# Kernel tuning notes

Measured on AMD Instinct MI355X. Metric: run time of the kernel, lower is better.

The kernel has to match this reference:

```python
import jax, jax.numpy as jnp
import numpy as np

NUM_SAMPLES = 50

def _sample_bezier(cp, t):
    # cp: [4, 2], t: [S, 1] -> [S, 2]
    p0, p1, p2, p3 = cp[0], cp[1], cp[2], cp[3]
    return ((1 - t) ** 3 * p0 + 3 * (1 - t) ** 2 * t * p1
            + 3 * (1 - t) * t ** 2 * p2 + t ** 3 * p3)

def setup_inputs() -> dict:
    key = jax.random.key(0)
    k1, k2, k3 = jax.random.split(key, 3)
    num_strokes = 64
    return {
        "strokes": jax.random.uniform(k1, (num_strokes, 4, 2), dtype=jnp.float32),
        "stroke_widths": jax.random.uniform(k2, (num_strokes,), dtype=jnp.float32) * 2.0 + 1.0,
        "stroke_colors": jax.random.uniform(k3, (num_strokes, 3), dtype=jnp.float32),
        "canvas_size": 512,
    }

def reference(strokes, stroke_widths, stroke_colors, canvas_size):
    H = W = canvas_size
    t = jnp.linspace(0.0, 1.0, NUM_SAMPLES, dtype=strokes.dtype)[:, None]  # [S,1]
    # sample all curves: [num_strokes, S, 2], scaled to pixel coords
    points = jax.vmap(lambda cp: _sample_bezier(cp, t))(strokes) * canvas_size
    coords = jnp.arange(canvas_size, dtype=strokes.dtype)
    yy, xx = jnp.meshgrid(coords, coords, indexing="ij")
    grid = jnp.stack([xx, yy], axis=-1)  # [H, W, 2]

    def composite(canvas, inp):
        pts, width, color = inp  # [S,2], [], [3]
        diff = grid[:, :, None, :] - pts[None, None, :, :]      # [H, W, S, 2]
        dist = jnp.sqrt(jnp.sum(diff * diff, axis=-1))           # [H, W, S]
        min_dist = jnp.min(dist, axis=-1)                        # [H, W]
        alpha = jax.nn.sigmoid((width - min_dist) * 2.0)         # [H, W]
        alpha = alpha[None, None]                                # [1,1,H,W]
        color_map = color[None, :, None, None]                   # [1,3,1,1]
        canvas = canvas * (1.0 - alpha) + color_map * alpha
        return canvas, None

    canvas0 = jnp.ones((1, 3, H, W), dtype=strokes.dtype)
    canvas, _ = jax.lax.scan(composite, canvas0, (points, stroke_widths, stroke_colors))
    return canvas
```

## Files before the change

kernel.cpp:

```cpp
#include <hip/hip_runtime.h>

#define NSTROKES 64
#define NSAMP    50
#define CANVAS   512
#define HW       (CANVAS * CANVAS)
#define TPB      1024
#define SPW      (NSTROKES / 16)
#define LSTRIDE  64

__global__ __launch_bounds__(TPB, 8) void raster_fused_kernel(
    const float* __restrict__ strokes,
    const float* __restrict__ widths,
    const float* __restrict__ colors,
    float* __restrict__ out)
{
    __shared__ __align__(16) float2 slist[NSTROKES * LSTRIDE];
    __shared__ float4 scull[NSTROKES];
    __shared__ float4 scol [NSTROKES];

    const int tid  = threadIdx.x;
    const int wave = tid >> 6;
    const int lane = tid & 63;
    const int px   = tid & 511;
    const int grp  = tid >> 9;
    const int y    = blockIdx.x;
    const float fy = (float)y;

    #pragma unroll
    for (int i = 0; i < SPW; ++i) {
        const int s = wave * SPW + i;

        float4 a = ((const float4*)strokes)[s * 2];
        float4 b = ((const float4*)strokes)[s * 2 + 1];
        const float S = (float)CANVAS;
        float c0x = a.x * S;
        float c1x = 3.0f * (a.z - a.x) * S;
        float c2x = 3.0f * (b.x - 2.0f * a.z + a.x) * S;
        float c3x = (b.z - 3.0f * b.x + 3.0f * a.z - a.x) * S;
        float c0y = a.y * S;
        float c1y = 3.0f * (a.w - a.y) * S;
        float c2y = 3.0f * (b.y - 2.0f * a.w + a.y) * S;
        float c3y = (b.w - 3.0f * b.y + 3.0f * a.w - a.y) * S;

        float w   = widths[s];
        float cut = w + 10.0f;

        float t   = (float)lane * (1.0f / (float)(NSAMP - 1));
        float px_ = fmaf(fmaf(fmaf(c3x, t, c2x), t, c1x), t, c0x);
        float py_ = fmaf(fmaf(fmaf(c3y, t, c2y), t, c1y), t, c0y);

        bool keep = (lane < NSAMP) && (fabsf(py_ - fy) <= cut);
        unsigned long long mask = __ballot(keep);
        int idx = __popcll(mask & ((1ull << lane) - 1ull));
        if (keep) {
            slist[s * LSTRIDE + idx] = make_float2(px_, py_);
        } else if (lane >= NSAMP) {
            slist[s * LSTRIDE + idx + (lane - NSAMP)] = make_float2(1e15f, 1e15f);
        }

        if (mask) {
            float vmn = keep ? px_ : 1e30f;
            float vmx = keep ? px_ : -1e30f;
            #pragma unroll
            for (int off = 32; off; off >>= 1) {
                vmn = fminf(vmn, __shfl_xor(vmn, off));
                vmx = fmaxf(vmx, __shfl_xor(vmx, off));
            }
            if (lane == 0) {
                scull[s] = make_float4(vmn - cut, vmx + cut, w,
                                       (float)__popcll(mask));
                scol [s] = make_float4(colors[3*s], colors[3*s+1],
                                       colors[3*s+2], 0.0f);
            }
        } else if (lane == 0) {
            scull[s] = make_float4(0.0f, 0.0f, w, 0.0f);
        }
    }
    __syncthreads();

    const float fx      = (float)px;
    const float span_lo = (float)((wave & 7) << 6);
    const float span_hi = span_lo + 63.0f;
    const int   sbase   = grp << 5;

    float4 cbl = scull[sbase + (lane & 31)];
    bool alive = (cbl.w > 0.0f) && (cbl.x <= span_hi) && (cbl.y >= span_lo);
    unsigned int live = (unsigned int)__ballot(alive);

    float A = 1.0f, br = 0.0f, bg = 0.0f, bb = 0.0f;

    while (live) {
        const int s0 = sbase + (__ffs(live) - 1);
        live &= live - 1u;
        const bool has1 = (live != 0u);
        const int s1 = has1 ? (sbase + (__ffs(live) - 1)) : s0;
        if (has1) live &= live - 1u;

        float4 cb0  = scull[s0];
        float4 cb1  = scull[s1];
        float4 col0 = scol [s0];
        float4 col1 = scol [s1];
        const int   kc0 = (int)cb0.w;
        const int   kc1 = has1 ? (int)cb1.w : 0;
        const float w0  = cb0.z;
        const float w1  = cb1.z;

        float m0 = 1e30f, m1 = 1e30f;
        const float4* L0 = (const float4*)(slist + s0 * LSTRIDE);
        const float4* L1 = (const float4*)(slist + s1 * LSTRIDE);

        const int kmax = kc0 > kc1 ? kc0 : kc1;
        for (int j = 0; j < kmax; j += 4) {
            if (j < kc0) {
                float4 q0 = L0[(j >> 1)];
                float4 q1 = L0[(j >> 1) + 1];
                float dy0 = fy - q0.y, dy1 = fy - q0.w;
                float dy2 = fy - q1.y, dy3 = fy - q1.w;
                float d0  = fx - q0.x, d1  = fx - q0.z;
                float d2  = fx - q1.x, d3  = fx - q1.z;
                float a01 = fminf(fmaf(d0, d0, dy0*dy0), fmaf(d1, d1, dy1*dy1));
                float a23 = fminf(fmaf(d2, d2, dy2*dy2), fmaf(d3, d3, dy3*dy3));
                m0 = fminf(fminf(a01, a23), m0);
            }
            if (j < kc1) {
                float4 q0 = L1[(j >> 1)];
                float4 q1 = L1[(j >> 1) + 1];
                float dy0 = fy - q0.y, dy1 = fy - q0.w;
                float dy2 = fy - q1.y, dy3 = fy - q1.w;
                float d0  = fx - q0.x, d1  = fx - q0.z;
                float d2  = fx - q1.x, d3  = fx - q1.z;
                float a01 = fminf(fmaf(d0, d0, dy0*dy0), fmaf(d1, d1, dy1*dy1));
                float a23 = fminf(fmaf(d2, d2, dy2*dy2), fmaf(d3, d3, dy3*dy3));
                m1 = fminf(fminf(a01, a23), m1);
            }
        }

        float al0 = __builtin_amdgcn_rcpf(1.0f + __expf(2.0f * (sqrtf(m0) - w0)));
        float al1 = __builtin_amdgcn_rcpf(1.0f + __expf(2.0f * (sqrtf(m1) - w1)));

        A  *= (1.0f - al0);
        br  = fmaf(al0, col0.x - br, br);
        bg  = fmaf(al0, col0.y - bg, bg);
        bb  = fmaf(al0, col0.z - bb, bb);
        if (has1) {
            A  *= (1.0f - al1);
            br  = fmaf(al1, col1.x - br, br);
            bg  = fmaf(al1, col1.y - bg, bg);
            bb  = fmaf(al1, col1.z - bb, bb);
        }
    }

    __syncthreads();
    float4* xfer = (float4*)slist;
    if (grp == 0) {
        xfer[px] = make_float4(A, br, bg, bb);
    }
    __syncthreads();
    if (grp == 1) {
        float4 g0 = xfer[px];
        float cr = fmaf(A, g0.x + g0.y, br);
        float cg = fmaf(A, g0.x + g0.z, bg);
        float cb = fmaf(A, g0.x + g0.w, bb);
        const int base = y * CANVAS + px;
        out[0*HW + base] = cr;
        out[1*HW + base] = cg;
        out[2*HW + base] = cb;
    }
}

extern "C" void kernel_launch(void* const* d_in, const int* in_sizes, int n_in,
                              void* d_out, int out_size, void* d_ws, size_t ws_size,
                              hipStream_t stream) {
    const float* strokes = (const float*)d_in[0];
    const float* widths  = (const float*)d_in[1];
    const float* colors  = (const float*)d_in[2];
    float* out = (float*)d_out;

    raster_fused_kernel<<<dim3(CANVAS), dim3(TPB), 0, stream>>>(
        strokes, widths, colors, out);
}
```

Measured before the change: 18.08 us.

## Bucket kept curve samples by x-span so each wave scans only nearby buckets

```diff
diff --git a/kernel.cpp b/kernel.cpp
--- a/kernel.cpp
+++ b/kernel.cpp
@@ -7,6 +7,7 @@
 #define TPB      1024
 #define SPW      (NSTROKES / 16)
 #define LSTRIDE  64
+#define SOFFP    13
 
 __global__ __launch_bounds__(TPB, 8) void raster_fused_kernel(
     const float* __restrict__ strokes,
@@ -15,8 +16,8 @@
     float* __restrict__ out)
 {
     __shared__ __align__(16) float2 slist[NSTROKES * LSTRIDE];
-    __shared__ float4 scull[NSTROKES];
-    __shared__ float4 scol [NSTROKES];
+    __shared__ unsigned int soff[NSTROKES * SOFFP];
+    __shared__ float4 scol[NSTROKES];
 
     const int tid  = threadIdx.x;
     const int wave = tid >> 6;
@@ -50,42 +51,58 @@
         float py_ = fmaf(fmaf(fmaf(c3y, t, c2y), t, c1y), t, c0y);
 
         bool keep = (lane < NSAMP) && (fabsf(py_ - fy) <= cut);
-        unsigned long long mask = __ballot(keep);
-        int idx = __popcll(mask & ((1ull << lane) - 1ull));
+
+        int bkt = (int)px_ >> 6;
+        bkt = bkt < 0 ? 0 : (bkt > 7 ? 7 : bkt);
+
+        unsigned long long mymask = 0ull;
+        unsigned int cnts[8];
+        #pragma unroll
+        for (int bb = 0; bb < 8; ++bb) {
+            unsigned long long mb = __ballot(keep && (bkt == bb));
+            mymask = (bkt == bb) ? mb : mymask;
+            cnts[bb] = (unsigned int)__popcll(mb);
+        }
+        unsigned int offs[9];
+        offs[0] = 0;
+        #pragma unroll
+        for (int bb = 0; bb < 8; ++bb) offs[bb + 1] = offs[bb] + cnts[bb];
+        const unsigned int kc = offs[8];
+
+        unsigned int myoff = offs[0];
+        #pragma unroll
+        for (int bb = 1; bb < 8; ++bb) myoff = (bkt == bb) ? offs[bb] : myoff;
+        int myidx = __popcll(mymask & ((1ull << lane) - 1ull));
+
         if (keep) {
-            slist[s * LSTRIDE + idx] = make_float2(px_, py_);
+            slist[s * LSTRIDE + myoff + myidx] = make_float2(px_, py_);
         } else if (lane >= NSAMP) {
-            slist[s * LSTRIDE + idx + (lane - NSAMP)] = make_float2(1e15f, 1e15f);
+            slist[s * LSTRIDE + kc + (lane - NSAMP)] = make_float2(1e15f, 1e15f);
         }
 
-        if (mask) {
-            float vmn = keep ? px_ : 1e30f;
-            float vmx = keep ? px_ : -1e30f;
+        if (lane < 9) {
+            unsigned int v = offs[0];
             #pragma unroll
-            for (int off = 32; off; off >>= 1) {
-                vmn = fminf(vmn, __shfl_xor(vmn, off));
-                vmx = fmaxf(vmx, __shfl_xor(vmx, off));
-            }
-            if (lane == 0) {
-                scull[s] = make_float4(vmn - cut, vmx + cut, w,
-                                       (float)__popcll(mask));
-                scol [s] = make_float4(colors[3*s], colors[3*s+1],
-                                       colors[3*s+2], 0.0f);
-            }
-        } else if (lane == 0) {
-            scull[s] = make_float4(0.0f, 0.0f, w, 0.0f);
+            for (int bb = 1; bb < 9; ++bb) v = (lane == bb) ? offs[bb] : v;
+            soff[s * SOFFP + lane] = v;
         }
+        if (lane == 0)
+            scol[s] = make_float4(colors[3*s], colors[3*s+1], colors[3*s+2], w);
     }
     __syncthreads();
 
-    const float fx      = (float)px;
-    const float span_lo = (float)((wave & 7) << 6);
-    const float span_hi = span_lo + 63.0f;
-    const int   sbase   = grp << 5;
+    const float fx  = (float)px;
+    const int   sg  = wave & 7;
+    const int   blo = sg > 0 ? sg - 1 : 0;
+    const int   bhi = (sg < 7 ? sg + 1 : 7) + 1;
+    const int   sbase = grp << 5;
 
-    float4 cbl = scull[sbase + (lane & 31)];
-    bool alive = (cbl.w > 0.0f) && (cbl.x <= span_hi) && (cbl.y >= span_lo);
-    unsigned int live = (unsigned int)__ballot(alive);
+    {
+    }
+    const int ls = sbase + (lane & 31);
+    unsigned int st_l = soff[ls * SOFFP + blo];
+    unsigned int en_l = soff[ls * SOFFP + bhi];
+    unsigned int live = (unsigned int)__ballot(en_l > st_l);
 
     float A = 1.0f, br = 0.0f, bg = 0.0f, bb = 0.0f;
 
@@ -96,24 +113,24 @@
         const int s1 = has1 ? (sbase + (__ffs(live) - 1)) : s0;
         if (has1) live &= live - 1u;
 
-        float4 cb0  = scull[s0];
-        float4 cb1  = scull[s1];
-        float4 col0 = scol [s0];
-        float4 col1 = scol [s1];
-        const int   kc0 = (int)cb0.w;
-        const int   kc1 = has1 ? (int)cb1.w : 0;
-        const float w0  = cb0.z;
-        const float w1  = cb1.z;
+        const int j0 = (int)(soff[s0 * SOFFP + blo] & ~3u);
+        const int e0 = (int)soff[s0 * SOFFP + bhi];
+        const int j1 = (int)(soff[s1 * SOFFP + blo] & ~3u);
+        const int e1 = has1 ? (int)soff[s1 * SOFFP + bhi] : 0;
+        float4 col0 = scol[s0];
+        float4 col1 = scol[s1];
+        const float w0 = col0.w, w1 = col1.w;
 
         float m0 = 1e30f, m1 = 1e30f;
         const float4* L0 = (const float4*)(slist + s0 * LSTRIDE);
         const float4* L1 = (const float4*)(slist + s1 * LSTRIDE);
 
-        const int kmax = kc0 > kc1 ? kc0 : kc1;
-        for (int j = 0; j < kmax; j += 4) {
-            if (j < kc0) {
-                float4 q0 = L0[(j >> 1)];
-                float4 q1 = L0[(j >> 1) + 1];
+        const int n0 = e0 - j0, n1 = e1 - j1;
+        const int n  = n0 > n1 ? n0 : n1;
+        for (int o = 0; o < n; o += 4) {
+            if (o < n0) {
+                float4 q0 = L0[(j0 + o) >> 1];
+                float4 q1 = L0[((j0 + o) >> 1) + 1];
                 float dy0 = fy - q0.y, dy1 = fy - q0.w;
                 float dy2 = fy - q1.y, dy3 = fy - q1.w;
                 float d0  = fx - q0.x, d1  = fx - q0.z;
@@ -122,9 +139,9 @@
                 float a23 = fminf(fmaf(d2, d2, dy2*dy2), fmaf(d3, d3, dy3*dy3));
                 m0 = fminf(fminf(a01, a23), m0);
             }
-            if (j < kc1) {
-                float4 q0 = L1[(j >> 1)];
-                float4 q1 = L1[(j >> 1) + 1];
+            if (o < n1) {
+                float4 q0 = L1[(j1 + o) >> 1];
+                float4 q1 = L1[((j1 + o) >> 1) + 1];
                 float dy0 = fy - q0.y, dy1 = fy - q0.w;
                 float dy2 = fy - q1.y, dy3 = fy - q1.w;
                 float d0  = fx - q0.x, d1  = fx - q0.z;
```

Result: slower. 21.12 us (+16.8%).

## Split per-row curve sampling into separate kernel and halve raster block size

Applied to the files above, without the earlier changes.

```diff
diff --git a/kernel.cpp b/kernel.cpp
--- a/kernel.cpp
+++ b/kernel.cpp
@@ -4,13 +4,65 @@
 #define NSAMP    50
 #define CANVAS   512
 #define HW       (CANVAS * CANVAS)
-#define TPB      1024
-#define SPW      (NSTROKES / 16)
 #define LSTRIDE  64
 
-__global__ __launch_bounds__(TPB, 8) void raster_fused_kernel(
+#define WS_LIST_BYTES ((size_t)CANVAS * NSTROKES * LSTRIDE * sizeof(float2))
+#define WS_NEED       (WS_LIST_BYTES + (size_t)CANVAS * NSTROKES * sizeof(float4))
+
+__global__ __launch_bounds__(256) void sample_kernel(
     const float* __restrict__ strokes,
     const float* __restrict__ widths,
+    float2* __restrict__ ws_list,
+    float4* __restrict__ ws_hdr)
+{
+    const int t   = blockIdx.x * 256 + threadIdx.x;
+    const int row = t >> 6;
+    const int s   = t & 63;
+    const float fy = (float)row;
+
+    float4 a = ((const float4*)strokes)[s * 2];
+    float4 b = ((const float4*)strokes)[s * 2 + 1];
+    const float S = (float)CANVAS;
+    float c0x = a.x * S;
+    float c1x = 3.0f * (a.z - a.x) * S;
+    float c2x = 3.0f * (b.x - 2.0f * a.z + a.x) * S;
+    float c3x = (b.z - 3.0f * b.x + 3.0f * a.z - a.x) * S;
+    float c0y = a.y * S;
+    float c1y = 3.0f * (a.w - a.y) * S;
+    float c2y = 3.0f * (b.y - 2.0f * a.w + a.y) * S;
+    float c3y = (b.w - 3.0f * b.y + 3.0f * a.w - a.y) * S;
+
+    float w   = widths[s];
+    float cut = w + 10.0f;
+
+    float2* L = ws_list + ((size_t)row * NSTROKES + s) * LSTRIDE;
+    int cnt = 0;
+    float xmn = 1e30f, xmx = -1e30f;
+
+    #pragma unroll 10
+    for (int j = 0; j < NSAMP; ++j) {
+        float tt = (float)j * (1.0f / (float)(NSAMP - 1));
+        float px = fmaf(fmaf(fmaf(c3x, tt, c2x), tt, c1x), tt, c0x);
+        float py = fmaf(fmaf(fmaf(c3y, tt, c2y), tt, c1y), tt, c0y);
+        if (fabsf(py - fy) <= cut) {
+            L[cnt] = make_float2(px, py);
+            ++cnt;
+            xmn = fminf(xmn, px);
+            xmx = fmaxf(xmx, px);
+        }
+    }
+    L[cnt]     = make_float2(1e15f, 1e15f);
+    L[cnt + 1] = make_float2(1e15f, 1e15f);
+    L[cnt + 2] = make_float2(1e15f, 1e15f);
+    L[cnt + 3] = make_float2(1e15f, 1e15f);
+
+    ws_hdr[row * NSTROKES + s] =
+        make_float4(xmn - cut, xmx + cut, w, (float)cnt);
+}
+
+__global__ __launch_bounds__(512, 8) void raster_kernel(
+    const float2* __restrict__ ws_list,
+    const float4* __restrict__ ws_hdr,
     const float* __restrict__ colors,
     float* __restrict__ out)
 {
@@ -21,65 +73,26 @@
     const int tid  = threadIdx.x;
     const int wave = tid >> 6;
     const int lane = tid & 63;
-    const int px   = tid & 511;
-    const int grp  = tid >> 9;
-    const int y    = blockIdx.x;
-    const float fy = (float)y;
-
+    const int pxl  = tid & 255;
+    const int grp  = tid >> 8;
+    const int row  = blockIdx.x >> 1;
+    const int half = blockIdx.x & 1;
+    const float fy = (float)row;
+
+    const size_t rbase = (size_t)row * NSTROKES;
     #pragma unroll
-    for (int i = 0; i < SPW; ++i) {
-        const int s = wave * SPW + i;
-
-        float4 a = ((const float4*)strokes)[s * 2];
-        float4 b = ((const float4*)strokes)[s * 2 + 1];
-        const float S = (float)CANVAS;
-        float c0x = a.x * S;
-        float c1x = 3.0f * (a.z - a.x) * S;
-        float c2x = 3.0f * (b.x - 2.0f * a.z + a.x) * S;
-        float c3x = (b.z - 3.0f * b.x + 3.0f * a.z - a.x) * S;
-        float c0y = a.y * S;
-        float c1y = 3.0f * (a.w - a.y) * S;
-        float c2y = 3.0f * (b.y - 2.0f * a.w + a.y) * S;
-        float c3y = (b.w - 3.0f * b.y + 3.0f * a.w - a.y) * S;
-
-        float w   = widths[s];
-        float cut = w + 10.0f;
-
-        float t   = (float)lane * (1.0f / (float)(NSAMP - 1));
-        float px_ = fmaf(fmaf(fmaf(c3x, t, c2x), t, c1x), t, c0x);
-        float py_ = fmaf(fmaf(fmaf(c3y, t, c2y), t, c1y), t, c0y);
-
-        bool keep = (lane < NSAMP) && (fabsf(py_ - fy) <= cut);
-        unsigned long long mask = __ballot(keep);
-        int idx = __popcll(mask & ((1ull << lane) - 1ull));
-        if (keep) {
-            slist[s * LSTRIDE + idx] = make_float2(px_, py_);
-        } else if (lane >= NSAMP) {
-            slist[s * LSTRIDE + idx + (lane - NSAMP)] = make_float2(1e15f, 1e15f);
-        }
-
-        if (mask) {
-            float vmn = keep ? px_ : 1e30f;
-            float vmx = keep ? px_ : -1e30f;
-            #pragma unroll
-            for (int off = 32; off; off >>= 1) {
-                vmn = fminf(vmn, __shfl_xor(vmn, off));
-                vmx = fmaxf(vmx, __shfl_xor(vmx, off));
-            }
-            if (lane == 0) {
-                scull[s] = make_float4(vmn - cut, vmx + cut, w,
-                                       (float)__popcll(mask));
-                scol [s] = make_float4(colors[3*s], colors[3*s+1],
-                                       colors[3*s+2], 0.0f);
-            }
-        } else if (lane == 0) {
-            scull[s] = make_float4(0.0f, 0.0f, w, 0.0f);
-        }
-    }
-    __syncthreads();
-
-    const float fx      = (float)px;
-    const float span_lo = (float)((wave & 7) << 6);
+    for (int i = 0; i < 8; ++i) {
+        const int s = wave * 8 + i;
+        slist[s * LSTRIDE + lane] = ws_list[(rbase + s) * LSTRIDE + lane];
+    }
+    if (lane < 8) scull[wave * 8 + lane] = ws_hdr[rbase + wave * 8 + lane];
+    if (tid < NSTROKES)
+        scol[tid] = make_float4(colors[3*tid], colors[3*tid+1],
+                                colors[3*tid+2], 0.0f);
+    __syncthreads();
+
+    const float fx      = (float)(half * 256 + pxl);
+    const float span_lo = (float)(half * 256 + ((wave & 3) << 6));
     const float span_hi = span_lo + 63.0f;
     const int   sbase   = grp << 5;
 
@@ -153,6 +166,163 @@
     __syncthreads();
     float4* xfer = (float4*)slist;
     if (grp == 0) {
+        xfer[pxl] = make_float4(A, br, bg, bb);
+    }
+    __syncthreads();
+    if (grp == 1) {
+        float4 g0 = xfer[pxl];
+        float cr = fmaf(A, g0.x + g0.y, br);
+        float cg = fmaf(A, g0.x + g0.z, bg);
+        float cb = fmaf(A, g0.x + g0.w, bb);
+        const int base = row * CANVAS + half * 256 + pxl;
+        out[0*HW + base] = cr;
+        out[1*HW + base] = cg;
+        out[2*HW + base] = cb;
+    }
+}
+
+__global__ __launch_bounds__(1024, 8) void raster_fused_fallback(
+    const float* __restrict__ strokes, const float* __restrict__ widths,
+    const float* __restrict__ colors, float* __restrict__ out)
+{
+    __shared__ __align__(16) float2 slist[NSTROKES * LSTRIDE];
+    __shared__ float4 scull[NSTROKES];
+    __shared__ float4 scol [NSTROKES];
+
+    const int tid  = threadIdx.x;
+    const int wave = tid >> 6;
+    const int lane = tid & 63;
+    const int px   = tid & 511;
+    const int grp  = tid >> 9;
+    const int y    = blockIdx.x;
+    const float fy = (float)y;
+
+    #pragma unroll
+    for (int i = 0; i < 4; ++i) {
+        const int s = wave * 4 + i;
+        float4 a = ((const float4*)strokes)[s * 2];
+        float4 b = ((const float4*)strokes)[s * 2 + 1];
+        const float S = (float)CANVAS;
+        float c0x = a.x * S;
+        float c1x = 3.0f * (a.z - a.x) * S;
+        float c2x = 3.0f * (b.x - 2.0f * a.z + a.x) * S;
+        float c3x = (b.z - 3.0f * b.x + 3.0f * a.z - a.x) * S;
+        float c0y = a.y * S;
+        float c1y = 3.0f * (a.w - a.y) * S;
+        float c2y = 3.0f * (b.y - 2.0f * a.w + a.y) * S;
+        float c3y = (b.w - 3.0f * b.y + 3.0f * a.w - a.y) * S;
+
+        float w   = widths[s];
+        float cut = w + 10.0f;
+
+        float t   = (float)lane * (1.0f / (float)(NSAMP - 1));
+        float px_ = fmaf(fmaf(fmaf(c3x, t, c2x), t, c1x), t, c0x);
+        float py_ = fmaf(fmaf(fmaf(c3y, t, c2y), t, c1y), t, c0y);
+
+        bool keep = (lane < NSAMP) && (fabsf(py_ - fy) <= cut);
+        unsigned long long mask = __ballot(keep);
+        int idx = __popcll(mask & ((1ull << lane) - 1ull));
+        if (keep) {
+            slist[s * LSTRIDE + idx] = make_float2(px_, py_);
+        } else if (lane >= NSAMP) {
+            slist[s * LSTRIDE + idx + (lane - NSAMP)] = make_float2(1e15f, 1e15f);
+        }
+
+        if (mask) {
+            float vmn = keep ? px_ : 1e30f;
+            float vmx = keep ? px_ : -1e30f;
+            #pragma unroll
+            for (int off = 32; off; off >>= 1) {
+                vmn = fminf(vmn, __shfl_xor(vmn, off));
+                vmx = fmaxf(vmx, __shfl_xor(vmx, off));
+            }
+            if (lane == 0) {
+                scull[s] = make_float4(vmn - cut, vmx + cut, w,
+                                       (float)__popcll(mask));
+                scol [s] = make_float4(colors[3*s], colors[3*s+1],
+                                       colors[3*s+2], 0.0f);
+            }
+        } else if (lane == 0) {
+            scull[s] = make_float4(0.0f, 0.0f, w, 0.0f);
+        }
+    }
+    __syncthreads();
+
+    const float fx      = (float)px;
+    const float span_lo = (float)((wave & 7) << 6);
+    const float span_hi = span_lo + 63.0f;
+    const int   sbase   = grp << 5;
+
+    float4 cbl = scull[sbase + (lane & 31)];
+    bool alive = (cbl.w > 0.0f) && (cbl.x <= span_hi) && (cbl.y >= span_lo);
+    unsigned int live = (unsigned int)__ballot(alive);
+
+    float A = 1.0f, br = 0.0f, bg = 0.0f, bb = 0.0f;
+
+    while (live) {
+        const int s0 = sbase + (__ffs(live) - 1);
+        live &= live - 1u;
+        const bool has1 = (live != 0u);
+        const int s1 = has1 ? (sbase + (__ffs(live) - 1)) : s0;
+        if (has1) live &= live - 1u;
+
+        float4 cb0  = scull[s0];
+        float4 cb1  = scull[s1];
+        float4 col0 = scol [s0];
+        float4 col1 = scol [s1];
+        const int   kc0 = (int)cb0.w;
+        const int   kc1 = has1 ? (int)cb1.w : 0;
+        const float w0  = cb0.z;
+        const float w1  = cb1.z;
+
+        float m0 = 1e30f, m1 = 1e30f;
+        const float4* L0 = (const float4*)(slist + s0 * LSTRIDE);
+        const float4* L1 = (const float4*)(slist + s1 * LSTRIDE);
+
+        const int kmax = kc0 > kc1 ? kc0 : kc1;
+        for (int j = 0; j < kmax; j += 4) {
+            if (j < kc0) {
+                float4 q0 = L0[(j >> 1)];
+                float4 q1 = L0[(j >> 1) + 1];
+                float dy0 = fy - q0.y, dy1 = fy - q0.w;
+                float dy2 = fy - q1.y, dy3 = fy - q1.w;
+                float d0  = fx - q0.x, d1  = fx - q0.z;
+                float d2  = fx - q1.x, d3  = fx - q1.z;
+                float a01 = fminf(fmaf(d0, d0, dy0*dy0), fmaf(d1, d1, dy1*dy1));
+                float a23 = fminf(fmaf(d2, d2, dy2*dy2), fmaf(d3, d3, dy3*dy3));
+                m0 = fminf(fminf(a01, a23), m0);
+            }
+            if (j < kc1) {
+                float4 q0 = L1[(j >> 1)];
+                float4 q1 = L1[(j >> 1) + 1];
+                float dy0 = fy - q0.y, dy1 = fy - q0.w;
+                float dy2 = fy - q1.y, dy3 = fy - q1.w;
+                float d0  = fx - q0.x, d1  = fx - q0.z;
+                float d2  = fx - q1.x, d3  = fx - q1.z;
+                float a01 = fminf(fmaf(d0, d0, dy0*dy0), fmaf(d1, d1, dy1*dy1));
+                float a23 = fminf(fmaf(d2, d2, dy2*dy2), fmaf(d3, d3, dy3*dy3));
+                m1 = fminf(fminf(a01, a23), m1);
+            }
+        }
+
+        float al0 = __builtin_amdgcn_rcpf(1.0f + __expf(2.0f * (sqrtf(m0) - w0)));
+        float al1 = __builtin_amdgcn_rcpf(1.0f + __expf(2.0f * (sqrtf(m1) - w1)));
+
+        A  *= (1.0f - al0);
+        br  = fmaf(al0, col0.x - br, br);
+        bg  = fmaf(al0, col0.y - bg, bg);
+        bb  = fmaf(al0, col0.z - bb, bb);
+        if (has1) {
+            A  *= (1.0f - al1);
+            br  = fmaf(al1, col1.x - br, br);
+            bg  = fmaf(al1, col1.y - bg, bg);
+            bb  = fmaf(al1, col1.z - bb, bb);
+        }
+    }
+
+    __syncthreads();
+    float4* xfer = (float4*)slist;
+    if (grp == 0) {
         xfer[px] = make_float4(A, br, bg, bb);
     }
     __syncthreads();
@@ -176,6 +346,15 @@
     const float* colors  = (const float*)d_in[2];
     float* out = (float*)d_out;
 
-    raster_fused_kernel<<<dim3(CANVAS), dim3(TPB), 0, stream>>>(
-        strokes, widths, colors, out);
+    if (ws_size >= WS_NEED) {
+        float2* ws_list = (float2*)d_ws;
+        float4* ws_hdr  = (float4*)((char*)d_ws + WS_LIST_BYTES);
+        sample_kernel<<<dim3((CANVAS * NSTROKES) / 256), dim3(256), 0, stream>>>(
+            strokes, widths, ws_list, ws_hdr);
+        raster_kernel<<<dim3(CANVAS * 2), dim3(512), 0, stream>>>(
+            ws_list, ws_hdr, colors, out);
+    } else {
+        raster_fused_fallback<<<dim3(CANVAS), dim3(1024), 0, stream>>>(
+            strokes, widths, colors, out);
+    }
 }
```

After: 21.62 us. +19.6%, slower.
